# Kernel optimization log

Measured on AMD Instinct MI355X. Metric: run time of the kernel, lower is better.

Reference implementation:

```python
import jax, jax.numpy as jnp
import numpy as np

N, E, G = 50000, 800000, 64
DIN, HID, HEADS, L = 128, 128, 4, 3
CH = HID // HEADS  # 32
EPS = 1e-5


def seg_sum(d, ids, n):
    return jax.ops.segment_sum(d, ids, num_segments=n)


def seg_max(d, ids, n):
    return jax.ops.segment_max(d, ids, num_segments=n)


def seg_mean(d, ids, n):
    s = seg_sum(d, ids, n)
    c = seg_sum(jnp.ones((d.shape[0], 1), d.dtype), ids, n)
    return s / jnp.maximum(c, 1.0)


def setup_inputs() -> dict:
    key = jax.random.key(0)
    ks = jax.random.split(key, 24)
    p = lambda k, sh: jax.random.normal(k, sh, jnp.float32) * 0.05
    z = lambda *sh: jnp.zeros(sh, jnp.float32)
    return {
        'x': jax.random.normal(ks[0], (N, DIN), jnp.float32),
        'edge_index': jax.random.randint(ks[1], (2, E), 0, N),
        'batch': jnp.sort(jax.random.randint(ks[2], (N,), 0, G)),
        'proj_W': p(ks[3], (DIN, HID)), 'proj_b': z(HID),
        'gcn_W': p(ks[4], (L, HID, HID)), 'gcn_b': z(L, HID),
        'gat_W': p(ks[5], (L, HID, HID)),
        'gat_asrc': p(ks[6], (L, HEADS, CH)), 'gat_adst': p(ks[7], (L, HEADS, CH)),
        'gat_b': z(L, HID),
        'norm_w': jnp.ones((L, HID), jnp.float32), 'norm_b': z(L, HID),
        'norm_ms': jnp.ones((L, HID), jnp.float32),
        'hub_W1': p(ks[8], (HID, HID // 2)), 'hub_b1': z(HID // 2),
        'hub_W2': p(ks[9], (HID // 2, 4)), 'hub_b2': z(4),
        'att_W1': p(ks[10], (HID, HID // 2)), 'att_b1': z(HID // 2),
        'att_W2': p(ks[11], (HID // 2, 1)), 'att_b2': z(1),
        'pat_W1': p(ks[12], (HID * 2, HID)), 'pat_b1': z(HID),
        'pat_W2': p(ks[13], (HID, HID // 2)), 'pat_b2': z(HID // 2),
        'pat_W3': p(ks[14], (HID // 2, 8)), 'pat_b3': z(8),
        'cls_W1': p(ks[15], (HID + 12, HID)), 'cls_b1': z(HID),
        'cls_W2': p(ks[16], (HID, HID // 2)), 'cls_b2': z(HID // 2),
        'cls_W3': p(ks[17], (HID // 2, 2)), 'cls_b3': z(2),
    }


def _forward(fl, edge_index, batch):
    src, dst = edge_index[0], edge_index[1]
    loops = jnp.arange(N)
    s = jnp.concatenate([src, loops])  # with self-loops (GCN/GAT default)
    d = jnp.concatenate([dst, loops])

    x = fl['x'] @ fl['proj_W'] + fl['proj_b']  # [N, HID]

    # symmetric GCN normalization (shared across layers)
    deg = seg_sum(jnp.ones(s.shape[0], jnp.float32), d, N)
    dis = jnp.where(deg > 0, 1.0 / jnp.sqrt(deg), 0.0)
    coef = (dis[s] * dis[d])[:, None]  # [E+N, 1]

    for i in range(L):
        # GCNConv: out[dst] += norm * (x @ W)[src]
        h_gcn = seg_sum((x @ fl['gcn_W'][i])[s] * coef, d, N) + fl['gcn_b'][i]
        # GATConv (heads=4, concat), eval mode (no dropout)
        hh = (x @ fl['gat_W'][i]).reshape(N, HEADS, CH)
        a_s = (hh * fl['gat_asrc'][i]).sum(-1)  # [N, HEADS]
        a_d = (hh * fl['gat_adst'][i]).sum(-1)
        e = jax.nn.leaky_relu(a_s[s] + a_d[d], negative_slope=0.2)  # [E+N, HEADS]
        e = jnp.exp(e - seg_max(e, d, N)[d])
        alpha = e / seg_sum(e, d, N)[d]
        h_gat = seg_sum(hh[s] * alpha[:, :, None], d, N).reshape(N, HID) + fl['gat_b'][i]
        h = h_gcn + h_gat
        # GraphNorm: per-graph, per-feature
        mean = seg_mean(h, batch, G)
        out = h - fl['norm_ms'][i] * mean[batch]
        var = seg_mean(out * out, batch, G)
        out = out / jnp.sqrt(var[batch] + EPS)
        h = jax.nn.relu(fl['norm_w'][i] * out + fl['norm_b'][i])
        x = h if i == 0 else x + h

    # hub importance: normalized max degree per graph == 1.0 iff any degree > 0
    ones_e = jnp.ones(E, jnp.float32)
    node_deg = seg_sum(ones_e, src, N) + seg_sum(ones_e, dst, N)
    max_deg = seg_max(node_deg, batch, G)
    hub_importance = (max_deg > 0).astype(jnp.float32)

    hub_feat = jax.nn.relu(x @ fl['hub_W1'] + fl['hub_b1']) @ fl['hub_W2'] + fl['hub_b2']
    hub_pooled = seg_mean(hub_feat, batch, G)  # [G, 4]

    # attention pooling: softmax over ALL nodes (dim=0), then per-graph weighted sum
    w = jax.nn.relu(x @ fl['att_W1'] + fl['att_b1']) @ fl['att_W2'] + fl['att_b2']  # [N,1]
    w = jax.nn.softmax(w, axis=0)
    graph_emb = seg_sum(x * w, batch, G)  # [G, HID]

    pattern_emb = jnp.concatenate([seg_mean(x, batch, G), seg_max(x, batch, G)], axis=1)
    pf = jax.nn.relu(pattern_emb @ fl['pat_W1'] + fl['pat_b1'])
    pf = jax.nn.relu(pf @ fl['pat_W2'] + fl['pat_b2'])
    pattern_features = pf @ fl['pat_W3'] + fl['pat_b3']  # [G, 8]

    comb = jnp.concatenate([graph_emb, hub_pooled, pattern_features], axis=1)
    c = jax.nn.relu(comb @ fl['cls_W1'] + fl['cls_b1'])
    c = jax.nn.relu(c @ fl['cls_W2'] + fl['cls_b2'])
    logits = c @ fl['cls_W3'] + fl['cls_b3']  # [G, 2]
    return logits, hub_importance, graph_emb, hub_pooled, pattern_features


def reference(x, edge_index, batch, proj_W, proj_b, gcn_W, gcn_b, gat_W, gat_asrc,
              gat_adst, gat_b, norm_w, norm_b, norm_ms, hub_W1, hub_b1, hub_W2,
              hub_b2, att_W1, att_b1, att_W2, att_b2, pat_W1, pat_b1, pat_W2,
              pat_b2, pat_W3, pat_b3, cls_W1, cls_b1, cls_W2, cls_b2, cls_W3, cls_b3):
    fl = dict(x=x, proj_W=proj_W, proj_b=proj_b, gcn_W=gcn_W, gcn_b=gcn_b,
              gat_W=gat_W, gat_asrc=gat_asrc, gat_adst=gat_adst, gat_b=gat_b,
              norm_w=norm_w, norm_b=norm_b, norm_ms=norm_ms,
              hub_W1=hub_W1, hub_b1=hub_b1, hub_W2=hub_W2, hub_b2=hub_b2,
              att_W1=att_W1, att_b1=att_b1, att_W2=att_W2, att_b2=att_b2,
              pat_W1=pat_W1, pat_b1=pat_b1, pat_W2=pat_W2, pat_b2=pat_b2,
              pat_W3=pat_W3, pat_b3=pat_b3, cls_W1=cls_W1, cls_b1=cls_b1,
              cls_W2=cls_W2, cls_b2=cls_b2, cls_W3=cls_W3, cls_b3=cls_b3)
    return _forward(fl, edge_index, batch)
```

## Files before the change

### kernel.cpp

```cpp
#include <hip/hip_runtime.h>

#define NN 50000
#define NE 800000
#define NG 64
#define HID 128

typedef __attribute__((ext_vector_type(8))) short bf16x8;
typedef __attribute__((ext_vector_type(4))) float f32x4;

__device__ __forceinline__ unsigned short f2b(float f) {
  unsigned u = __float_as_uint(f);
  u += 0x7fffu + ((u >> 16) & 1u);
  return (unsigned short)(u >> 16);
}
__device__ __forceinline__ float b2f(unsigned short b) {
  return __uint_as_float(((unsigned)b) << 16);
}

__global__ void count_edges(const int* __restrict__ ei, int* __restrict__ cnt_dst,
                            int* __restrict__ cnt_src) {
  int e = blockIdx.x * 256 + threadIdx.x;
  if (e >= NE) return;
  atomicAdd(&cnt_src[ei[e]], 1);
  atomicAdd(&cnt_dst[ei[NE + e]], 1);
}

__global__ void compute_dis(const int* __restrict__ cnt_dst, float* __restrict__ dis) {
  int n = blockIdx.x * 256 + threadIdx.x;
  if (n >= NN) return;
  dis[n] = rsqrtf((float)(cnt_dst[n] + 1));
}

__global__ void scanA(const int* __restrict__ cnt, int* __restrict__ partial) {
  __shared__ int s[256];
  int t = threadIdx.x;
  int i = blockIdx.x * 256 + t;
  s[t] = (i < NN) ? cnt[i] : 0;
  __syncthreads();
  for (int off = 128; off; off >>= 1) {
    if (t < off) s[t] += s[t + off];
    __syncthreads();
  }
  if (!t) partial[blockIdx.x] = s[0];
}

__global__ void scanB(int* __restrict__ partial, int nb) {
  if (threadIdx.x == 0 && blockIdx.x == 0) {
    int acc = 0;
    for (int i = 0; i < nb; ++i) { int v = partial[i]; partial[i] = acc; acc += v; }
  }
}

__global__ void scanC(const int* __restrict__ cnt, const int* __restrict__ partial,
                      int* __restrict__ rowptr) {
  __shared__ int bufA[256], bufB[256];
  int t = threadIdx.x;
  int i = blockIdx.x * 256 + t;
  int v = (i < NN) ? cnt[i] : 0;
  bufA[t] = v;
  __syncthreads();
  int* src = bufA; int* dst = bufB;
  for (int off = 1; off < 256; off <<= 1) {
    int x = src[t];
    if (t >= off) x += src[t - off];
    dst[t] = x;
    __syncthreads();
    int* tmp = src; src = dst; dst = tmp;
  }
  int incl = src[t];
  if (i < NN) rowptr[i] = partial[blockIdx.x] + incl - v;
  if (i == NN - 1) rowptr[NN] = partial[blockIdx.x] + incl;
}

__global__ void fill_edges(const int* __restrict__ ei, const int* __restrict__ rowptr,
                           int* __restrict__ fillpos, int* __restrict__ col) {
  int e = blockIdx.x * 256 + threadIdx.x;
  if (e >= NE) return;
  int s = ei[e], d = ei[NE + e];
  int p = atomicAdd(&fillpos[d], 1);
  col[rowptr[d] + p] = s;
}

__global__ void graph_bounds(const int* __restrict__ batch, int* __restrict__ gstart) {
  int g = threadIdx.x;
  if (g > NG) return;
  int lo = 0, hi = NN;
  while (lo < hi) { int mid = (lo + hi) >> 1; if (batch[mid] < g) lo = mid + 1; else hi = mid; }
  gstart[g] = lo;
}

__global__ void prep_wfrag(const float* __restrict__ gcn_W, const float* __restrict__ gat_W,
                           unsigned short* __restrict__ F) {
  int l = blockIdx.y;
  int idx = blockIdx.x * 256 + threadIdx.x;
  int j = idx & 7, lane = (idx >> 3) & 63, t = idx >> 9;
  int ct = t >> 2, ks = t & 3;
  int k = ks * 32 + ((lane >> 4) << 3) + j;
  int c = (ct << 4) + (lane & 15);
  const float* W1 = gcn_W + (size_t)l * 16384;
  const float* W2 = gat_W + (size_t)l * 16384;
  F[(size_t)l * 32768 + idx] = f2b(W1[k * 128 + c]);
  F[(size_t)l * 32768 + 16384 + idx] = f2b(W2[k * 128 + c]);
}

__global__ void prep_frag1(const float* __restrict__ W, unsigned short* __restrict__ F) {
  int idx = blockIdx.x * 256 + threadIdx.x;
  int j = idx & 7, lane = (idx >> 3) & 63, t = idx >> 9;
  int ct = t >> 2, ks = t & 3;
  int k = ks * 32 + ((lane >> 4) << 3) + j;
  int c = (ct << 4) + (lane & 15);
  F[idx] = f2b(W[k * 128 + c]);
}

__global__ void prep_nodefrag(const float* __restrict__ hW1, const float* __restrict__ aW1,
                              unsigned short* __restrict__ F) {
  int idx = blockIdx.x * 256 + threadIdx.x;
  int j = idx & 7, lane = (idx >> 3) & 63, t = idx >> 9;
  int ct = t >> 2, ks = t & 3;
  int k = ks * 32 + ((lane >> 4) << 3) + j;
  int c = (ct << 4) + (lane & 15);
  float v = (c < 64) ? hW1[k * 64 + c] : aW1[k * 64 + (c - 64)];
  F[idx] = f2b(v);
}

__device__ __forceinline__ void load_a_frags(const float* __restrict__ xp, int lane,
                                             bf16x8 a[4]) {
#pragma unroll
  for (int ks = 0; ks < 4; ++ks) {
    int k0 = ks * 32 + ((lane >> 4) << 3);
    float4 u = *(const float4*)&xp[k0];
    float4 v = *(const float4*)&xp[k0 + 4];
    bf16x8 t;
    t[0] = (short)f2b(u.x); t[1] = (short)f2b(u.y); t[2] = (short)f2b(u.z); t[3] = (short)f2b(u.w);
    t[4] = (short)f2b(v.x); t[5] = (short)f2b(v.y); t[6] = (short)f2b(v.z); t[7] = (short)f2b(v.w);
    a[ks] = t;
  }
}

__global__ __launch_bounds__(256) void gemm_proj_mfma(
    const float* __restrict__ X, const unsigned short* __restrict__ F,
    const float* __restrict__ bias, float* __restrict__ Y, int nrows) {
  __shared__ float Ys[64 * 128];
  int tid = threadIdx.x;
  int w = tid >> 6, lane = tid & 63;
  int row0 = blockIdx.x * 64;
  int row = row0 + w * 16 + (lane & 15);
  const float* xp = (row < nrows) ? &X[(size_t)row * 128] : &X[0];
  bf16x8 a[4];
  load_a_frags(xp, lane, a);
  f32x4 acc[8];
#pragma unroll
  for (int ct = 0; ct < 8; ++ct) acc[ct] = (f32x4){0.f, 0.f, 0.f, 0.f};
#pragma unroll
  for (int ct = 0; ct < 8; ++ct) {
#pragma unroll
    for (int ks = 0; ks < 4; ++ks) {
      bf16x8 b = *(const bf16x8*)&F[((ct * 4 + ks) * 64 + lane) * 8];
      acc[ct] = __builtin_amdgcn_mfma_f32_16x16x32_bf16(a[ks], b, acc[ct], 0, 0, 0);
    }
  }
#pragma unroll
  for (int ct = 0; ct < 8; ++ct) {
    int c = (ct << 4) + (lane & 15);
    float bv = bias[c];
#pragma unroll
    for (int j = 0; j < 4; ++j) {
      int r = w * 16 + ((lane >> 4) << 2) + j;
      Ys[r * 128 + c] = acc[ct][j] + bv;
    }
  }
  __syncthreads();
  int nr = min(nrows - row0, 64);
  const float4* ys4 = (const float4*)Ys;
  float4* y4 = (float4*)(Y + (size_t)row0 * 128);
  for (int e = tid; e < nr * 32; e += 256) y4[e] = ys4[e];
}

__global__ __launch_bounds__(256) void gemm_dual_mfma(
    const float* __restrict__ X, const unsigned short* __restrict__ F1,
    const unsigned short* __restrict__ F2, const float* __restrict__ asrc,
    const float* __restrict__ adst, unsigned short* __restrict__ G,
    float* __restrict__ a_s, float* __restrict__ a_d, int nrows) {
  __shared__ unsigned short Gs[64 * 256];
  int tid = threadIdx.x;
  int w = tid >> 6, lane = tid & 63;
  int row0 = blockIdx.x * 64;
  int row = row0 + w * 16 + (lane & 15);
  const float* xp = (row < nrows) ? &X[(size_t)row * 128] : &X[0];
  bf16x8 a[4];
  load_a_frags(xp, lane, a);
  f32x4 acc1[8], acc2[8];
#pragma unroll
  for (int ct = 0; ct < 8; ++ct) {
    acc1[ct] = (f32x4){0.f, 0.f, 0.f, 0.f};
    acc2[ct] = (f32x4){0.f, 0.f, 0.f, 0.f};
  }
#pragma unroll
  for (int ct = 0; ct < 8; ++ct) {
#pragma unroll
    for (int ks = 0; ks < 4; ++ks) {
      int off = ((ct * 4 + ks) * 64 + lane) * 8;
      bf16x8 b1 = *(const bf16x8*)&F1[off];
      bf16x8 b2 = *(const bf16x8*)&F2[off];
      acc1[ct] = __builtin_amdgcn_mfma_f32_16x16x32_bf16(a[ks], b1, acc1[ct], 0, 0, 0);
      acc2[ct] = __builtin_amdgcn_mfma_f32_16x16x32_bf16(a[ks], b2, acc2[ct], 0, 0, 0);
    }
  }
#pragma unroll
  for (int ct = 0; ct < 8; ++ct) {
#pragma unroll
    for (int j = 0; j < 4; ++j) {
      int r = w * 16 + ((lane >> 4) << 2) + j;
      int c = (ct << 4) + (lane & 15);
      Gs[r * 256 + c] = f2b(acc1[ct][j]);
      Gs[r * 256 + 128 + c] = f2b(acc2[ct][j]);
    }
  }
  __syncthreads();
  int nr = min(nrows - row0, 64);
  const uint4* gs4 = (const uint4*)Gs;
  uint4* g4 = (uint4*)(G + (size_t)row0 * 256);
  for (int e = tid; e < nr * 32; e += 256) g4[e] = gs4[e];
  int f = 2 * lane;
  float as0 = asrc[f], as1 = asrc[f + 1];
  float ad0 = adst[f], ad1 = adst[f + 1];
  for (int i = 0; i < 16; ++i) {
    int r = w * 16 + i;
    int n = row0 + r;
    if (n >= nrows) break;
    ushort2 v = *(const ushort2*)&Gs[r * 256 + 128 + f];
    float x0 = b2f(v.x), x1 = b2f(v.y);
    float ps = x0 * as0 + x1 * as1;
    float pd = x0 * ad0 + x1 * ad1;
    ps += __shfl_xor(ps, 1); pd += __shfl_xor(pd, 1);
    ps += __shfl_xor(ps, 2); pd += __shfl_xor(pd, 2);
    ps += __shfl_xor(ps, 4); pd += __shfl_xor(pd, 4);
    ps += __shfl_xor(ps, 8); pd += __shfl_xor(pd, 8);
    if ((lane & 15) == 0) {
      int h = lane >> 4;
      a_s[n * 4 + h] = ps;
      a_d[n * 4 + h] = pd;
    }
  }
}

__global__ __launch_bounds__(256) void node_mlps_mfma(
    const float* __restrict__ x, const unsigned short* __restrict__ Fn,
    const float* __restrict__ hb1, const float* __restrict__ ab1,
    const float* __restrict__ hW2, const float* __restrict__ hb2,
    const float* __restrict__ aW2, const float* __restrict__ ab2,
    float* __restrict__ hub_feat, float* __restrict__ w_att) {
  __shared__ float Hs[64 * 133];
  int tid = threadIdx.x;
  int w = tid >> 6, lane = tid & 63;
  int row0 = blockIdx.x * 64;
  int row = row0 + w * 16 + (lane & 15);
  const float* xp = (row < NN) ? &x[(size_t)row * 128] : &x[0];
  bf16x8 a[4];
  load_a_frags(xp, lane, a);
  f32x4 acc[8];
#pragma unroll
  for (int ct = 0; ct < 8; ++ct) acc[ct] = (f32x4){0.f, 0.f, 0.f, 0.f};
#pragma unroll
  for (int ct = 0; ct < 8; ++ct) {
#pragma unroll
    for (int ks = 0; ks < 4; ++ks) {
      bf16x8 b = *(const bf16x8*)&Fn[((ct * 4 + ks) * 64 + lane) * 8];
      acc[ct] = __builtin_amdgcn_mfma_f32_16x16x32_bf16(a[ks], b, acc[ct], 0, 0, 0);
    }
  }
#pragma unroll
  for (int ct = 0; ct < 8; ++ct) {
    int c = (ct << 4) + (lane & 15);
    float bias = (c < 64) ? hb1[c] : ab1[c - 64];
#pragma unroll
    for (int j = 0; j < 4; ++j) {
      int r = w * 16 + ((lane >> 4) << 2) + j;
      float v = acc[ct][j] + bias;
      Hs[r * 133 + c] = v > 0.f ? v : 0.f;
    }
  }
  __syncthreads();
  int r = tid & 63, o = tid >> 6;
  int n = row0 + r;
  if (n < NN) {
    float d = hb2[o];
#pragma unroll 8
    for (int k = 0; k < 64; ++k) d += Hs[r * 133 + k] * hW2[k * 4 + o];
    hub_feat[n * 4 + o] = d;
    if (tid < 64) {
      float d2 = ab2[0];
#pragma unroll 8
      for (int k = 0; k < 64; ++k) d2 += Hs[r * 133 + 64 + k] * aW2[k];
      w_att[n] = d2;
    }
  }
}

__device__ __forceinline__ float lrelu(float v) { return v > 0.f ? v : 0.2f * v; }

__global__ __launch_bounds__(256) void edge_aggregate_p(
    const unsigned short* __restrict__ G, const float* __restrict__ a_s,
    const float* __restrict__ a_d, const float* __restrict__ dis,
    const int* __restrict__ rowptr, const int* __restrict__ col,
    const float* __restrict__ gcn_b, const float* __restrict__ gat_b,
    float* __restrict__ hout) {
  int n = blockIdx.x * 4 + (threadIdx.x >> 6);
  int lane = threadIdx.x & 63;
  int es = lane >> 4, fl = lane & 15;
  int h = fl >> 2;
  int f8 = fl << 3;
  int p0 = rowptr[n], p1 = rowptr[n + 1];
  int cnt = p1 - p0 + 1;
  float adh = a_d[n * 4 + h];
  float dn = dis[n];
  float ag[8] = {0.f, 0.f, 0.f, 0.f, 0.f, 0.f, 0.f, 0.f};
  float aa[8] = {0.f, 0.f, 0.f, 0.f, 0.f, 0.f, 0.f, 0.f};
  float ssum = 0.f;
#define EDGE_ACC(coef, eu, xv, hv)                          \
  do {                                                      \
    ag[0] += (coef)*__uint_as_float((xv).x << 16);          \
    ag[1] += (coef)*__uint_as_float((xv).x & 0xffff0000u);  \
    ag[2] += (coef)*__uint_as_float((xv).y << 16);          \
    ag[3] += (coef)*__uint_as_float((xv).y & 0xffff0000u);  \
    ag[4] += (coef)*__uint_as_float((xv).z << 16);          \
    ag[5] += (coef)*__uint_as_float((xv).z & 0xffff0000u);  \
    ag[6] += (coef)*__uint_as_float((xv).w << 16);          \
    ag[7] += (coef)*__uint_as_float((xv).w & 0xffff0000u);  \
    aa[0] += (eu)*__uint_as_float((hv).x << 16);            \
    aa[1] += (eu)*__uint_as_float((hv).x & 0xffff0000u);    \
    aa[2] += (eu)*__uint_as_float((hv).y << 16);            \
    aa[3] += (eu)*__uint_as_float((hv).y & 0xffff0000u);    \
    aa[4] += (eu)*__uint_as_float((hv).z << 16);            \
    aa[5] += (eu)*__uint_as_float((hv).z & 0xffff0000u);    \
    aa[6] += (eu)*__uint_as_float((hv).w << 16);            \
    aa[7] += (eu)*__uint_as_float((hv).w & 0xffff0000u);    \
  } while (0)
  int e = es;
  for (; e + 4 < cnt; e += 8) {
    int eB = e + 4;
    int srcA = (e < cnt - 1) ? col[p0 + e] : n;
    int srcB = (eB < cnt - 1) ? col[p0 + eB] : n;
    float coefA = dis[srcA] * dn, coefB = dis[srcB] * dn;
    float euA = __expf(lrelu(a_s[srcA * 4 + h] + adh));
    float euB = __expf(lrelu(a_s[srcB * 4 + h] + adh));
    uint4 xvA = *(const uint4*)&G[(size_t)srcA * 256 + f8];
    uint4 hvA = *(const uint4*)&G[(size_t)srcA * 256 + 128 + f8];
    uint4 xvB = *(const uint4*)&G[(size_t)srcB * 256 + f8];
    uint4 hvB = *(const uint4*)&G[(size_t)srcB * 256 + 128 + f8];
    ssum += euA + euB;
    EDGE_ACC(coefA, euA, xvA, hvA);
    EDGE_ACC(coefB, euB, xvB, hvB);
  }
  for (; e < cnt; e += 4) {
    int src = (e < cnt - 1) ? col[p0 + e] : n;
    float coef = dis[src] * dn;
    float eu = __expf(lrelu(a_s[src * 4 + h] + adh));
    uint4 xv = *(const uint4*)&G[(size_t)src * 256 + f8];
    uint4 hv = *(const uint4*)&G[(size_t)src * 256 + 128 + f8];
    ssum += eu;
    EDGE_ACC(coef, eu, xv, hv);
  }
#undef EDGE_ACC
#pragma unroll
  for (int j = 0; j < 8; ++j) {
    ag[j] += __shfl_xor(ag[j], 16); ag[j] += __shfl_xor(ag[j], 32);
    aa[j] += __shfl_xor(aa[j], 16); aa[j] += __shfl_xor(aa[j], 32);
  }
  ssum += __shfl_xor(ssum, 16); ssum += __shfl_xor(ssum, 32);
  if (es == 0) {
    float rs = 1.f / ssum;
    float4 gb0 = *(const float4*)&gcn_b[f8];
    float4 gb1 = *(const float4*)&gcn_b[f8 + 4];
    float4 tb0 = *(const float4*)&gat_b[f8];
    float4 tb1 = *(const float4*)&gat_b[f8 + 4];
    float4 o0, o1;
    o0.x = ag[0] + aa[0] * rs + gb0.x + tb0.x;
    o0.y = ag[1] + aa[1] * rs + gb0.y + tb0.y;
    o0.z = ag[2] + aa[2] * rs + gb0.z + tb0.z;
    o0.w = ag[3] + aa[3] * rs + gb0.w + tb0.w;
    o1.x = ag[4] + aa[4] * rs + gb1.x + tb1.x;
    o1.y = ag[5] + aa[5] * rs + gb1.y + tb1.y;
    o1.z = ag[6] + aa[6] * rs + gb1.z + tb1.z;
    o1.w = ag[7] + aa[7] * rs + gb1.w + tb1.w;
    *(float4*)&hout[n * 128 + f8] = o0;
    *(float4*)&hout[n * 128 + f8 + 4] = o1;
  }
}

__global__ __launch_bounds__(128) void graph_stats_par(
    const float* __restrict__ h, const int* __restrict__ batch,
    float* __restrict__ S1, float* __restrict__ S2) {
  int f = threadIdx.x;
  int n0 = blockIdx.x * 64;
  int n1 = min(n0 + 64, NN);
  int g = batch[n0];
  float s1 = 0.f, s2 = 0.f;
  for (int n = n0; n < n1; ++n) {
    int gn = batch[n];
    if (gn != g) {
      atomicAdd(&S1[g * 128 + f], s1);
      atomicAdd(&S2[g * 128 + f], s2);
      s1 = 0.f; s2 = 0.f; g = gn;
    }
    float v = h[n * 128 + f];
    s1 += v; s2 += v * v;
  }
  atomicAdd(&S1[g * 128 + f], s1);
  atomicAdd(&S2[g * 128 + f], s2);
}

__global__ __launch_bounds__(256) void graph_norm(
    const float* __restrict__ h, const int* __restrict__ batch,
    const int* __restrict__ gstart, const float* __restrict__ S1,
    const float* __restrict__ S2, const float* __restrict__ nw,
    const float* __restrict__ nb, const float* __restrict__ nms,
    float* __restrict__ x, int layer) {
  int idx = blockIdx.x * 256 + threadIdx.x;
  if (idx >= NN * 32) return;
  int n = idx >> 5, fq = (idx & 31) << 2;
  int g = batch[n];
  float c = fmaxf((float)(gstart[g + 1] - gstart[g]), 1.f);
  float rc = 1.f / c;
  float4 s1 = *(const float4*)&S1[g * 128 + fq];
  float4 s2 = *(const float4*)&S2[g * 128 + fq];
  float4 ms = *(const float4*)&nms[fq];
  float4 w = *(const float4*)&nw[fq];
  float4 b = *(const float4*)&nb[fq];
  float4 hv = *(const float4*)&h[(size_t)n * 128 + fq];
  float4 o;
#define GN1(X)                                                           \
  {                                                                      \
    float mean = s1.X * rc;                                              \
    float var = s2.X * rc - mean * mean * ms.X * (2.f - ms.X);           \
    var = fmaxf(var, 0.f);                                               \
    float ot = (hv.X - ms.X * mean) * rsqrtf(var + 1e-5f);               \
    float t = w.X * ot + b.X;                                            \
    o.X = t > 0.f ? t : 0.f;                                             \
  }
  GN1(x) GN1(y) GN1(z) GN1(w)
#undef GN1
  float4* xp = (float4*)&x[(size_t)n * 128 + fq];
  if (layer == 0) {
    *xp = o;
  } else {
    float4 xo = *xp;
    xo.x += o.x; xo.y += o.y; xo.z += o.z; xo.w += o.w;
    *xp = xo;
  }
}

__global__ void reduce_max1(const float* __restrict__ w, float* __restrict__ tmpM) {
  __shared__ float s[256];
  int t = threadIdx.x;
  float m = -1e30f;
  for (int i = blockIdx.x * 256 + t; i < NN; i += gridDim.x * 256) m = fmaxf(m, w[i]);
  s[t] = m;
  __syncthreads();
  for (int off = 128; off; off >>= 1) {
    if (t < off) s[t] = fmaxf(s[t], s[t + off]);
    __syncthreads();
  }
  if (!t) tmpM[blockIdx.x] = s[0];
}

__global__ void reduce_max2(const float* __restrict__ tmpM, float* __restrict__ scal) {
  __shared__ float s[256];
  int t = threadIdx.x;
  s[t] = tmpM[t];
  __syncthreads();
  for (int off = 128; off; off >>= 1) {
    if (t < off) s[t] = fmaxf(s[t], s[t + off]);
    __syncthreads();
  }
  if (!t) scal[0] = s[0];
}

__global__ void reduce_sum1(const float* __restrict__ w, const float* __restrict__ scal,
                            float* __restrict__ tmpS) {
  __shared__ float s[256];
  int t = threadIdx.x;
  float gmax = scal[0];
  float acc = 0.f;
  for (int i = blockIdx.x * 256 + t; i < NN; i += gridDim.x * 256) acc += __expf(w[i] - gmax);
  s[t] = acc;
  __syncthreads();
  for (int off = 128; off; off >>= 1) {
    if (t < off) s[t] += s[t + off];
    __syncthreads();
  }
  if (!t) tmpS[blockIdx.x] = s[0];
}

__global__ void reduce_sum2(const float* __restrict__ tmpS, float* __restrict__ scal) {
  __shared__ float s[256];
  int t = threadIdx.x;
  s[t] = tmpS[t];
  __syncthreads();
  for (int off = 128; off; off >>= 1) {
    if (t < off) s[t] += s[t + off];
    __syncthreads();
  }
  if (!t) scal[1] = s[0];
}

__global__ __launch_bounds__(128) void graph_pool_par(
    const float* __restrict__ x, const float* __restrict__ hub_feat,
    const float* __restrict__ w_att, const int* __restrict__ batch,
    const float* __restrict__ scal, float* __restrict__ Sx,
    unsigned* __restrict__ Mx, float* __restrict__ WSx, float* __restrict__ Shub) {
  int f = threadIdx.x;
  int n0 = blockIdx.x * 64;
  int n1 = min(n0 + 64, NN);
  float gmax = scal[0];
  int g = batch[n0];
  float sx = 0.f, wx = 0.f, mx = 0.f, sh = 0.f;
  for (int n = n0; n < n1; ++n) {
    int gn = batch[n];
    if (gn != g) {
      atomicAdd(&Sx[g * 128 + f], sx);
      atomicAdd(&WSx[g * 128 + f], wx);
      atomicMax(&Mx[g * 128 + f], __float_as_uint(mx));
      if (f < 4) atomicAdd(&Shub[g * 4 + f], sh);
      sx = 0.f; wx = 0.f; mx = 0.f; sh = 0.f; g = gn;
    }
    float xv = x[n * 128 + f];
    float ew = __expf(w_att[n] - gmax);
    sx += xv;
    wx += ew * xv;
    mx = fmaxf(mx, xv);
    if (f < 4) sh += hub_feat[n * 4 + f];
  }
  atomicAdd(&Sx[g * 128 + f], sx);
  atomicAdd(&WSx[g * 128 + f], wx);
  atomicMax(&Mx[g * 128 + f], __float_as_uint(mx));
  if (f < 4) atomicAdd(&Shub[g * 4 + f], sh);
}

__global__ __launch_bounds__(128) void finalize(
    const float* __restrict__ Sx, const float* __restrict__ Mx,
    const float* __restrict__ WSx, const float* __restrict__ Shub,
    const float* __restrict__ scal, const int* __restrict__ gstart,
    const int* __restrict__ cnt_src, const int* __restrict__ cnt_dst,
    const float* __restrict__ pW1, const float* __restrict__ pb1,
    const float* __restrict__ pW2, const float* __restrict__ pb2,
    const float* __restrict__ pW3, const float* __restrict__ pb3,
    const float* __restrict__ cW1, const float* __restrict__ cb1,
    const float* __restrict__ cW2, const float* __restrict__ cb2,
    const float* __restrict__ cW3, const float* __restrict__ cb3,
    float* __restrict__ out) {
  int g = blockIdx.x, t = threadIdx.x;
  __shared__ float pe[256], comb[140], buf1[128], buf2[64];
  __shared__ int snd[128];
  int s = gstart[g], e = gstart[g + 1];
  float c = fmaxf((float)(e - s), 1.f);
  int mdeg = 0;
  for (int n = s + t; n < e; n += 128) mdeg = max(mdeg, cnt_src[n] + cnt_dst[n]);
  snd[t] = mdeg;
  float* out_logits = out;
  float* out_hub = out + 128;
  float* out_ge = out + 192;
  float* out_hp = out + 192 + 8192;
  float* out_pf = out + 192 + 8192 + 256;
  float ge = WSx[g * 128 + t] / scal[1];
  out_ge[g * 128 + t] = ge;
  comb[t] = ge;
  pe[t] = Sx[g * 128 + t] / c;
  pe[128 + t] = Mx[g * 128 + t];
  if (t < 4) {
    float hp = Shub[g * 4 + t] / c;
    out_hp[g * 4 + t] = hp;
    comb[128 + t] = hp;
  }
  __syncthreads();
  for (int off = 64; off; off >>= 1) {
    if (t < off) snd[t] = max(snd[t], snd[t + off]);
    __syncthreads();
  }
  if (t == 0) out_hub[g] = (snd[0] > 0) ? 1.f : 0.f;
  float v = pb1[t];
  for (int k = 0; k < 256; ++k) v += pe[k] * pW1[k * 128 + t];
  buf1[t] = v > 0.f ? v : 0.f;
  __syncthreads();
  if (t < 64) {
    float v2 = pb2[t];
    for (int k = 0; k < 128; ++k) v2 += buf1[k] * pW2[k * 64 + t];
    buf2[t] = v2 > 0.f ? v2 : 0.f;
  }
  __syncthreads();
  if (t < 8) {
    float v3 = pb3[t];
    for (int k = 0; k < 64; ++k) v3 += buf2[k] * pW3[k * 8 + t];
    out_pf[g * 8 + t] = v3;
    comb[132 + t] = v3;
  }
  __syncthreads();
  float u = cb1[t];
  for (int k = 0; k < 140; ++k) u += comb[k] * cW1[k * 128 + t];
  buf1[t] = u > 0.f ? u : 0.f;
  __syncthreads();
  if (t < 64) {
    float u2 = cb2[t];
    for (int k = 0; k < 128; ++k) u2 += buf1[k] * cW2[k * 64 + t];
    buf2[t] = u2 > 0.f ? u2 : 0.f;
  }
  __syncthreads();
  if (t < 2) {
    float u3 = cb3[t];
    for (int k = 0; k < 64; ++k) u3 += buf2[k] * cW3[k * 2 + t];
    out_logits[g * 2 + t] = u3;
  }
}

extern "C" void kernel_launch(void* const* d_in, const int* in_sizes, int n_in,
                              void* d_out, int out_size, void* d_ws, size_t ws_size,
                              hipStream_t stream) {
  const float* x_in = (const float*)d_in[0];
  const int* ei = (const int*)d_in[1];
  const int* batch = (const int*)d_in[2];
  const float* proj_W = (const float*)d_in[3];
  const float* proj_b = (const float*)d_in[4];
  const float* gcn_W = (const float*)d_in[5];
  const float* gcn_b = (const float*)d_in[6];
  const float* gat_W = (const float*)d_in[7];
  const float* gat_as = (const float*)d_in[8];
  const float* gat_ad = (const float*)d_in[9];
  const float* gat_b = (const float*)d_in[10];
  const float* norm_w = (const float*)d_in[11];
  const float* norm_b = (const float*)d_in[12];
  const float* norm_ms = (const float*)d_in[13];
  const float* hub_W1 = (const float*)d_in[14];
  const float* hub_b1 = (const float*)d_in[15];
  const float* hub_W2 = (const float*)d_in[16];
  const float* hub_b2 = (const float*)d_in[17];
  const float* att_W1 = (const float*)d_in[18];
  const float* att_b1 = (const float*)d_in[19];
  const float* att_W2 = (const float*)d_in[20];
  const float* att_b2 = (const float*)d_in[21];
  const float* pat_W1 = (const float*)d_in[22];
  const float* pat_b1 = (const float*)d_in[23];
  const float* pat_W2 = (const float*)d_in[24];
  const float* pat_b2 = (const float*)d_in[25];
  const float* pat_W3 = (const float*)d_in[26];
  const float* pat_b3 = (const float*)d_in[27];
  const float* cls_W1 = (const float*)d_in[28];
  const float* cls_b1 = (const float*)d_in[29];
  const float* cls_W2 = (const float*)d_in[30];
  const float* cls_b2 = (const float*)d_in[31];
  const float* cls_W3 = (const float*)d_in[32];
  const float* cls_b3 = (const float*)d_in[33];
  float* out = (float*)d_out;

  char* ws = (char*)d_ws;
  auto fbuf = [&](size_t n) { float* p = (float*)ws; ws += ((n * 4 + 255) / 256) * 256; return p; };
  auto ibuf = [&](size_t n) { int* p = (int*)ws; ws += ((n * 4 + 255) / 256) * 256; return p; };

  float* x = fbuf((size_t)NN * 128);
  unsigned short* gath = (unsigned short*)fbuf((size_t)NN * 128);
  float* h = fbuf((size_t)NN * 128);
  unsigned short* wfrag = (unsigned short*)fbuf(3 * 32768 / 2);
  unsigned short* nfrag = (unsigned short*)fbuf(16384 / 2);
  unsigned short* pfrag = (unsigned short*)fbuf(16384 / 2);
  float* a_s = fbuf((size_t)NN * 4);
  float* a_d = fbuf((size_t)NN * 4);
  float* dis = fbuf(NN);
  float* w_att = fbuf(NN);
  float* hub_feat = fbuf((size_t)NN * 4);
  float* S1 = fbuf(NG * 128);
  float* S2 = fbuf(NG * 128);
  float* Sx = fbuf(NG * 128);
  float* Mx = fbuf(NG * 128);
  float* WSx = fbuf(NG * 128);
  float* Shub = fbuf(NG * 4);
  float* tmpM = fbuf(256);
  float* tmpS = fbuf(256);
  float* scal = fbuf(4);
  int* zero0 = ibuf(3 * NN);
  int* cnt_dst = zero0;
  int* cnt_src = zero0 + NN;
  int* fillpos = zero0 + 2 * NN;
  int* rowptr = ibuf(NN + 1);
  int* col = ibuf(NE);
  int* partial = ibuf(256);
  int* gstart = ibuf(NG + 1);

  const int NB = (NN + 255) / 256;
  const int NC = (NN + 63) / 64;
  const int GM = (NN + 63) / 64;

  hipMemsetAsync(zero0, 0, (size_t)3 * NN * 4, stream);
  count_edges<<<NE / 256, 256, 0, stream>>>(ei, cnt_dst, cnt_src);
  compute_dis<<<NB, 256, 0, stream>>>(cnt_dst, dis);
  scanA<<<NB, 256, 0, stream>>>(cnt_dst, partial);
  scanB<<<1, 64, 0, stream>>>(partial, NB);
  scanC<<<NB, 256, 0, stream>>>(cnt_dst, partial, rowptr);
  fill_edges<<<NE / 256, 256, 0, stream>>>(ei, rowptr, fillpos, col);
  graph_bounds<<<1, 128, 0, stream>>>(batch, gstart);
  prep_wfrag<<<dim3(64, 3), 256, 0, stream>>>(gcn_W, gat_W, wfrag);
  prep_nodefrag<<<64, 256, 0, stream>>>(hub_W1, att_W1, nfrag);
  prep_frag1<<<64, 256, 0, stream>>>(proj_W, pfrag);

  gemm_proj_mfma<<<GM, 256, 0, stream>>>(x_in, pfrag, proj_b, x, NN);

  for (int l = 0; l < 3; ++l) {
    gemm_dual_mfma<<<GM, 256, 0, stream>>>(x, wfrag + (size_t)l * 32768,
                                           wfrag + (size_t)l * 32768 + 16384,
                                           gat_as + l * 128, gat_ad + l * 128,
                                           gath, a_s, a_d, NN);
    edge_aggregate_p<<<NN / 4, 256, 0, stream>>>(gath, a_s, a_d, dis, rowptr, col,
                                                 gcn_b + l * 128, gat_b + l * 128, h);
    hipMemsetAsync(S1, 0, (size_t)2 * NG * 128 * 4, stream);
    graph_stats_par<<<NC, 128, 0, stream>>>(h, batch, S1, S2);
    graph_norm<<<(NN * 32 + 255) / 256, 256, 0, stream>>>(h, batch, gstart, S1, S2,
                                                          norm_w + l * 128, norm_b + l * 128,
                                                          norm_ms + l * 128, x, l);
  }

  node_mlps_mfma<<<GM, 256, 0, stream>>>(x, nfrag, hub_b1, att_b1, hub_W2, hub_b2,
                                         att_W2, att_b2, hub_feat, w_att);

  reduce_max1<<<256, 256, 0, stream>>>(w_att, tmpM);
  reduce_max2<<<1, 256, 0, stream>>>(tmpM, scal);
  reduce_sum1<<<256, 256, 0, stream>>>(w_att, scal, tmpS);
  reduce_sum2<<<1, 256, 0, stream>>>(tmpS, scal);

  hipMemsetAsync(Sx, 0, (size_t)(3 * NG * 128 + NG * 4) * 4, stream);
  graph_pool_par<<<NC, 128, 0, stream>>>(x, hub_feat, w_att, batch, scal,
                                         Sx, (unsigned*)Mx, WSx, Shub);

  finalize<<<NG, 128, 0, stream>>>(Sx, Mx, WSx, Shub, scal, gstart, cnt_src, cnt_dst,
                                   pat_W1, pat_b1, pat_W2, pat_b2, pat_W3, pat_b3,
                                   cls_W1, cls_b1, cls_W2, cls_b2, cls_W3, cls_b3, out);
}
```

Before: 602.7 us.

## Fuse setup kernels, keep bf16 activations, prescale GCN by dis, drop softmax max

Merges the dis computation into the scan, graph bounds into the scan-B kernel, and the three weight-fragment prep kernels into one launch. Graph norm and projection also write a bf16 copy of x, which the MFMA GEMMs read directly instead of converting fp32. The source-side GCN normalization is applied in the GEMM epilogue, removing a per-edge dis gather. Memsets move into kernels, and the attention softmax max-reduction is removed, which risks overflow if attention logits grow large.

```diff
diff --git a/kernel.cpp b/kernel.cpp
--- a/kernel.cpp
+++ b/kernel.cpp
@@ -25,17 +25,14 @@
   atomicAdd(&cnt_dst[ei[NE + e]], 1);
 }
 
-__global__ void compute_dis(const int* __restrict__ cnt_dst, float* __restrict__ dis) {
-  int n = blockIdx.x * 256 + threadIdx.x;
-  if (n >= NN) return;
-  dis[n] = rsqrtf((float)(cnt_dst[n] + 1));
-}
-
-__global__ void scanA(const int* __restrict__ cnt, int* __restrict__ partial) {
+__global__ void scanA_dis(const int* __restrict__ cnt, int* __restrict__ partial,
+                          float* __restrict__ dis) {
   __shared__ int s[256];
   int t = threadIdx.x;
   int i = blockIdx.x * 256 + t;
-  s[t] = (i < NN) ? cnt[i] : 0;
+  int v = (i < NN) ? cnt[i] : 0;
+  if (i < NN) dis[i] = rsqrtf((float)(v + 1));
+  s[t] = v;
   __syncthreads();
   for (int off = 128; off; off >>= 1) {
     if (t < off) s[t] += s[t + off];
@@ -44,10 +41,18 @@
   if (!t) partial[blockIdx.x] = s[0];
 }
 
-__global__ void scanB(int* __restrict__ partial, int nb) {
-  if (threadIdx.x == 0 && blockIdx.x == 0) {
+__global__ void scanB_bounds(int* __restrict__ partial, int nb,
+                             const int* __restrict__ batch, int* __restrict__ gstart) {
+  int t = threadIdx.x;
+  if (t == 0) {
     int acc = 0;
     for (int i = 0; i < nb; ++i) { int v = partial[i]; partial[i] = acc; acc += v; }
+  }
+  if (t >= 1 && t <= NG + 1) {
+    int g = t - 1;
+    int lo = 0, hi = NN;
+    while (lo < hi) { int mid = (lo + hi) >> 1; if (batch[mid] < g) lo = mid + 1; else hi = mid; }
+    gstart[g] = lo;
   }
 }
 
@@ -81,50 +86,29 @@
   col[rowptr[d] + p] = s;
 }
 
-__global__ void graph_bounds(const int* __restrict__ batch, int* __restrict__ gstart) {
-  int g = threadIdx.x;
-  if (g > NG) return;
-  int lo = 0, hi = NN;
-  while (lo < hi) { int mid = (lo + hi) >> 1; if (batch[mid] < g) lo = mid + 1; else hi = mid; }
-  gstart[g] = lo;
-}
-
-__global__ void prep_wfrag(const float* __restrict__ gcn_W, const float* __restrict__ gat_W,
-                           unsigned short* __restrict__ F) {
-  int l = blockIdx.y;
+__global__ void prep_all(const float* __restrict__ gcn_W, const float* __restrict__ gat_W,
+                         const float* __restrict__ hW1, const float* __restrict__ aW1,
+                         const float* __restrict__ projW, unsigned short* __restrict__ wfrag,
+                         unsigned short* __restrict__ nfrag, unsigned short* __restrict__ pfrag) {
+  int m = blockIdx.y;
   int idx = blockIdx.x * 256 + threadIdx.x;
   int j = idx & 7, lane = (idx >> 3) & 63, t = idx >> 9;
   int ct = t >> 2, ks = t & 3;
   int k = ks * 32 + ((lane >> 4) << 3) + j;
   int c = (ct << 4) + (lane & 15);
-  const float* W1 = gcn_W + (size_t)l * 16384;
-  const float* W2 = gat_W + (size_t)l * 16384;
-  F[(size_t)l * 32768 + idx] = f2b(W1[k * 128 + c]);
-  F[(size_t)l * 32768 + 16384 + idx] = f2b(W2[k * 128 + c]);
-}
-
-__global__ void prep_frag1(const float* __restrict__ W, unsigned short* __restrict__ F) {
-  int idx = blockIdx.x * 256 + threadIdx.x;
-  int j = idx & 7, lane = (idx >> 3) & 63, t = idx >> 9;
-  int ct = t >> 2, ks = t & 3;
-  int k = ks * 32 + ((lane >> 4) << 3) + j;
-  int c = (ct << 4) + (lane & 15);
-  F[idx] = f2b(W[k * 128 + c]);
-}
-
-__global__ void prep_nodefrag(const float* __restrict__ hW1, const float* __restrict__ aW1,
-                              unsigned short* __restrict__ F) {
-  int idx = blockIdx.x * 256 + threadIdx.x;
-  int j = idx & 7, lane = (idx >> 3) & 63, t = idx >> 9;
-  int ct = t >> 2, ks = t & 3;
-  int k = ks * 32 + ((lane >> 4) << 3) + j;
-  int c = (ct << 4) + (lane & 15);
-  float v = (c < 64) ? hW1[k * 64 + c] : aW1[k * 64 + (c - 64)];
-  F[idx] = f2b(v);
-}
-
-__device__ __forceinline__ void load_a_frags(const float* __restrict__ xp, int lane,
-                                             bf16x8 a[4]) {
+  if (m < 3) {
+    wfrag[(size_t)m * 32768 + idx] = f2b(gcn_W[(size_t)m * 16384 + k * 128 + c]);
+    wfrag[(size_t)m * 32768 + 16384 + idx] = f2b(gat_W[(size_t)m * 16384 + k * 128 + c]);
+  } else if (m == 3) {
+    float v = (c < 64) ? hW1[k * 64 + c] : aW1[k * 64 + (c - 64)];
+    nfrag[idx] = f2b(v);
+  } else {
+    pfrag[idx] = f2b(projW[k * 128 + c]);
+  }
+}
+
+__device__ __forceinline__ void load_a_frags_f32(const float* __restrict__ xp, int lane,
+                                                 bf16x8 a[4]) {
 #pragma unroll
   for (int ks = 0; ks < 4; ++ks) {
     int k0 = ks * 32 + ((lane >> 4) << 3);
@@ -137,9 +121,19 @@
   }
 }
 
+__device__ __forceinline__ void load_a_frags_b16(const unsigned short* __restrict__ xp,
+                                                 int lane, bf16x8 a[4]) {
+#pragma unroll
+  for (int ks = 0; ks < 4; ++ks) {
+    int k0 = ks * 32 + ((lane >> 4) << 3);
+    a[ks] = *(const bf16x8*)&xp[k0];
+  }
+}
+
 __global__ __launch_bounds__(256) void gemm_proj_mfma(
     const float* __restrict__ X, const unsigned short* __restrict__ F,
-    const float* __restrict__ bias, float* __restrict__ Y, int nrows) {
+    const float* __restrict__ bias, float* __restrict__ Y,
+    unsigned short* __restrict__ YB, int nrows) {
   __shared__ float Ys[64 * 128];
   int tid = threadIdx.x;
   int w = tid >> 6, lane = tid & 63;
@@ -147,7 +141,7 @@
   int row = row0 + w * 16 + (lane & 15);
   const float* xp = (row < nrows) ? &X[(size_t)row * 128] : &X[0];
   bf16x8 a[4];
-  load_a_frags(xp, lane, a);
+  load_a_frags_f32(xp, lane, a);
   f32x4 acc[8];
 #pragma unroll
   for (int ct = 0; ct < 8; ++ct) acc[ct] = (f32x4){0.f, 0.f, 0.f, 0.f};
@@ -173,22 +167,30 @@
   int nr = min(nrows - row0, 64);
   const float4* ys4 = (const float4*)Ys;
   float4* y4 = (float4*)(Y + (size_t)row0 * 128);
-  for (int e = tid; e < nr * 32; e += 256) y4[e] = ys4[e];
+  ushort4* yb4 = (ushort4*)(YB + (size_t)row0 * 128);
+  for (int e = tid; e < nr * 32; e += 256) {
+    float4 v = ys4[e];
+    y4[e] = v;
+    ushort4 b;
+    b.x = f2b(v.x); b.y = f2b(v.y); b.z = f2b(v.z); b.w = f2b(v.w);
+    yb4[e] = b;
+  }
 }
 
 __global__ __launch_bounds__(256) void gemm_dual_mfma(
-    const float* __restrict__ X, const unsigned short* __restrict__ F1,
+    const unsigned short* __restrict__ XB, const unsigned short* __restrict__ F1,
     const unsigned short* __restrict__ F2, const float* __restrict__ asrc,
-    const float* __restrict__ adst, unsigned short* __restrict__ G,
-    float* __restrict__ a_s, float* __restrict__ a_d, int nrows) {
+    const float* __restrict__ adst, const float* __restrict__ dis,
+    unsigned short* __restrict__ G, float* __restrict__ a_s, float* __restrict__ a_d,
+    int nrows) {
   __shared__ unsigned short Gs[64 * 256];
   int tid = threadIdx.x;
   int w = tid >> 6, lane = tid & 63;
   int row0 = blockIdx.x * 64;
   int row = row0 + w * 16 + (lane & 15);
-  const float* xp = (row < nrows) ? &X[(size_t)row * 128] : &X[0];
+  const unsigned short* xp = (row < nrows) ? &XB[(size_t)row * 128] : &XB[0];
   bf16x8 a[4];
-  load_a_frags(xp, lane, a);
+  load_a_frags_b16(xp, lane, a);
   f32x4 acc1[8], acc2[8];
 #pragma unroll
   for (int ct = 0; ct < 8; ++ct) {
@@ -206,13 +208,19 @@
       acc2[ct] = __builtin_amdgcn_mfma_f32_16x16x32_bf16(a[ks], b2, acc2[ct], 0, 0, 0);
     }
   }
+  float dv[4];
+#pragma unroll
+  for (int j = 0; j < 4; ++j) {
+    int gr = row0 + w * 16 + ((lane >> 4) << 2) + j;
+    dv[j] = dis[gr < nrows ? gr : 0];
+  }
 #pragma unroll
   for (int ct = 0; ct < 8; ++ct) {
 #pragma unroll
     for (int j = 0; j < 4; ++j) {
       int r = w * 16 + ((lane >> 4) << 2) + j;
       int c = (ct << 4) + (lane & 15);
-      Gs[r * 256 + c] = f2b(acc1[ct][j]);
+      Gs[r * 256 + c] = f2b(acc1[ct][j] * dv[j]);
       Gs[r * 256 + 128 + c] = f2b(acc2[ct][j]);
     }
   }
@@ -245,7 +253,7 @@
 }
 
 __global__ __launch_bounds__(256) void node_mlps_mfma(
-    const float* __restrict__ x, const unsigned short* __restrict__ Fn,
+    const unsigned short* __restrict__ XB, const unsigned short* __restrict__ Fn,
     const float* __restrict__ hb1, const float* __restrict__ ab1,
     const float* __restrict__ hW2, const float* __restrict__ hb2,
     const float* __restrict__ aW2, const float* __restrict__ ab2,
@@ -255,9 +263,9 @@
   int w = tid >> 6, lane = tid & 63;
   int row0 = blockIdx.x * 64;
   int row = row0 + w * 16 + (lane & 15);
-  const float* xp = (row < NN) ? &x[(size_t)row * 128] : &x[0];
+  const unsigned short* xp = (row < NN) ? &XB[(size_t)row * 128] : &XB[0];
   bf16x8 a[4];
-  load_a_frags(xp, lane, a);
+  load_a_frags_b16(xp, lane, a);
   f32x4 acc[8];
 #pragma unroll
   for (int ct = 0; ct < 8; ++ct) acc[ct] = (f32x4){0.f, 0.f, 0.f, 0.f};
@@ -304,7 +312,10 @@
     const float* __restrict__ a_d, const float* __restrict__ dis,
     const int* __restrict__ rowptr, const int* __restrict__ col,
     const float* __restrict__ gcn_b, const float* __restrict__ gat_b,
-    float* __restrict__ hout) {
+    float* __restrict__ hout, float* __restrict__ S1z) {
+  if (blockIdx.x == 0) {
+    for (int i = threadIdx.x; i < 2 * NG * 128; i += 256) S1z[i] = 0.f;
+  }
   int n = blockIdx.x * 4 + (threadIdx.x >> 6);
   int lane = threadIdx.x & 63;
   int es = lane >> 4, fl = lane & 15;
@@ -317,16 +328,16 @@
   float ag[8] = {0.f, 0.f, 0.f, 0.f, 0.f, 0.f, 0.f, 0.f};
   float aa[8] = {0.f, 0.f, 0.f, 0.f, 0.f, 0.f, 0.f, 0.f};
   float ssum = 0.f;
-#define EDGE_ACC(coef, eu, xv, hv)                          \
+#define EDGE_ACC(eu, xv, hv)                                \
   do {                                                      \
-    ag[0] += (coef)*__uint_as_float((xv).x << 16);          \
-    ag[1] += (coef)*__uint_as_float((xv).x & 0xffff0000u);  \
-    ag[2] += (coef)*__uint_as_float((xv).y << 16);          \
-    ag[3] += (coef)*__uint_as_float((xv).y & 0xffff0000u);  \
-    ag[4] += (coef)*__uint_as_float((xv).z << 16);          \
-    ag[5] += (coef)*__uint_as_float((xv).z & 0xffff0000u);  \
-    ag[6] += (coef)*__uint_as_float((xv).w << 16);          \
-    ag[7] += (coef)*__uint_as_float((xv).w & 0xffff0000u);  \
+    ag[0] += __uint_as_float((xv).x << 16);                 \
+    ag[1] += __uint_as_float((xv).x & 0xffff0000u);         \
+    ag[2] += __uint_as_float((xv).y << 16);                 \
+    ag[3] += __uint_as_float((xv).y & 0xffff0000u);         \
+    ag[4] += __uint_as_float((xv).z << 16);                 \
+    ag[5] += __uint_as_float((xv).z & 0xffff0000u);         \
+    ag[6] += __uint_as_float((xv).w << 16);                 \
+    ag[7] += __uint_as_float((xv).w & 0xffff0000u);         \
     aa[0] += (eu)*__uint_as_float((hv).x << 16);            \
     aa[1] += (eu)*__uint_as_float((hv).x & 0xffff0000u);    \
     aa[2] += (eu)*__uint_as_float((hv).y << 16);            \
@@ -341,7 +352,6 @@
     int eB = e + 4;
     int srcA = (e < cnt - 1) ? col[p0 + e] : n;
     int srcB = (eB < cnt - 1) ? col[p0 + eB] : n;
-    float coefA = dis[srcA] * dn, coefB = dis[srcB] * dn;
     float euA = __expf(lrelu(a_s[srcA * 4 + h] + adh));
     float euB = __expf(lrelu(a_s[srcB * 4 + h] + adh));
     uint4 xvA = *(const uint4*)&G[(size_t)srcA * 256 + f8];
@@ -349,17 +359,16 @@
     uint4 xvB = *(const uint4*)&G[(size_t)srcB * 256 + f8];
     uint4 hvB = *(const uint4*)&G[(size_t)srcB * 256 + 128 + f8];
     ssum += euA + euB;
-    EDGE_ACC(coefA, euA, xvA, hvA);
-    EDGE_ACC(coefB, euB, xvB, hvB);
+    EDGE_ACC(euA, xvA, hvA);
+    EDGE_ACC(euB, xvB, hvB);
   }
   for (; e < cnt; e += 4) {
     int src = (e < cnt - 1) ? col[p0 + e] : n;
-    float coef = dis[src] * dn;
     float eu = __expf(lrelu(a_s[src * 4 + h] + adh));
     uint4 xv = *(const uint4*)&G[(size_t)src * 256 + f8];
     uint4 hv = *(const uint4*)&G[(size_t)src * 256 + 128 + f8];
     ssum += eu;
-    EDGE_ACC(coef, eu, xv, hv);
+    EDGE_ACC(eu, xv, hv);
   }
 #undef EDGE_ACC
 #pragma unroll
@@ -375,14 +384,14 @@
     float4 tb0 = *(const float4*)&gat_b[f8];
     float4 tb1 = *(const float4*)&gat_b[f8 + 4];
     float4 o0, o1;
-    o0.x = ag[0] + aa[0] * rs + gb0.x + tb0.x;
-    o0.y = ag[1] + aa[1] * rs + gb0.y + tb0.y;
-    o0.z = ag[2] + aa[2] * rs + gb0.z + tb0.z;
-    o0.w = ag[3] + aa[3] * rs + gb0.w + tb0.w;
-    o1.x = ag[4] + aa[4] * rs + gb1.x + tb1.x;
-    o1.y = ag[5] + aa[5] * rs + gb1.y + tb1.y;
-    o1.z = ag[6] + aa[6] * rs + gb1.z + tb1.z;
-    o1.w = ag[7] + aa[7] * rs + gb1.w + tb1.w;
+    o0.x = ag[0] * dn + aa[0] * rs + gb0.x + tb0.x;
+    o0.y = ag[1] * dn + aa[1] * rs + gb0.y + tb0.y;
+    o0.z = ag[2] * dn + aa[2] * rs + gb0.z + tb0.z;
+    o0.w = ag[3] * dn + aa[3] * rs + gb0.w + tb0.w;
+    o1.x = ag[4] * dn + aa[4] * rs + gb1.x + tb1.x;
+    o1.y = ag[5] * dn + aa[5] * rs + gb1.y + tb1.y;
+    o1.z = ag[6] * dn + aa[6] * rs + gb1.z + tb1.z;
+    o1.w = ag[7] * dn + aa[7] * rs + gb1.w + tb1.w;
     *(float4*)&hout[n * 128 + f8] = o0;
     *(float4*)&hout[n * 128 + f8 + 4] = o1;
   }
@@ -415,7 +424,7 @@
     const int* __restrict__ gstart, const float* __restrict__ S1,
     const float* __restrict__ S2, const float* __restrict__ nw,
     const float* __restrict__ nb, const float* __restrict__ nms,
-    float* __restrict__ x, int layer) {
+    float* __restrict__ x, unsigned short* __restrict__ xb, int layer) {
   int idx = blockIdx.x * 256 + threadIdx.x;
   if (idx >= NN * 32) return;
   int n = idx >> 5, fq = (idx & 31) << 2;
@@ -441,48 +450,28 @@
   GN1(x) GN1(y) GN1(z) GN1(w)
 #undef GN1
   float4* xp = (float4*)&x[(size_t)n * 128 + fq];
+  float4 xo;
   if (layer == 0) {
-    *xp = o;
+    xo = o;
   } else {
-    float4 xo = *xp;
+    xo = *xp;
     xo.x += o.x; xo.y += o.y; xo.z += o.z; xo.w += o.w;
-    *xp = xo;
-  }
-}
-
-__global__ void reduce_max1(const float* __restrict__ w, float* __restrict__ tmpM) {
+  }
+  *xp = xo;
+  ushort4 bo;
+  bo.x = f2b(xo.x); bo.y = f2b(xo.y); bo.z = f2b(xo.z); bo.w = f2b(xo.w);
+  *(ushort4*)&xb[(size_t)n * 128 + fq] = bo;
+}
+
+__global__ void reduce_sum1(const float* __restrict__ w, float* __restrict__ tmpS,
+                            float* __restrict__ poolZ, int zcount) {
   __shared__ float s[256];
   int t = threadIdx.x;
-  float m = -1e30f;
-  for (int i = blockIdx.x * 256 + t; i < NN; i += gridDim.x * 256) m = fmaxf(m, w[i]);
-  s[t] = m;
-  __syncthreads();
-  for (int off = 128; off; off >>= 1) {
-    if (t < off) s[t] = fmaxf(s[t], s[t + off]);
-    __syncthreads();
-  }
-  if (!t) tmpM[blockIdx.x] = s[0];
-}
-
-__global__ void reduce_max2(const float* __restrict__ tmpM, float* __restrict__ scal) {
-  __shared__ float s[256];
-  int t = threadIdx.x;
-  s[t] = tmpM[t];
-  __syncthreads();
-  for (int off = 128; off; off >>= 1) {
-    if (t < off) s[t] = fmaxf(s[t], s[t + off]);
-    __syncthreads();
-  }
-  if (!t) scal[0] = s[0];
-}
-
-__global__ void reduce_sum1(const float* __restrict__ w, const float* __restrict__ scal,
-                            float* __restrict__ tmpS) {
-  __shared__ float s[256];
-  int t = threadIdx.x;
-  float gmax = scal[0];
+  if (blockIdx.x == 0) {
+    for (int i = t; i < zcount; i += 256) poolZ[i] = 0.f;
+  }
   float acc = 0.f;
-  for (int i = blockIdx.x * 256 + t; i < NN; i += gridDim.x * 256) acc += __expf(w[i] - gmax);
+  for (int i = blockIdx.x * 256 + t; i < NN; i += gridDim.x * 256) acc += __expf(w[i]);
   s[t] = acc;
   __syncthreads();
   for (int off = 128; off; off >>= 1) {
@@ -507,12 +496,11 @@
 __global__ __launch_bounds__(128) void graph_pool_par(
     const float* __restrict__ x, const float* __restrict__ hub_feat,
     const float* __restrict__ w_att, const int* __restrict__ batch,
-    const float* __restrict__ scal, float* __restrict__ Sx,
-    unsigned* __restrict__ Mx, float* __restrict__ WSx, float* __restrict__ Shub) {
+    float* __restrict__ Sx, unsigned* __restrict__ Mx, float* __restrict__ WSx,
+    float* __restrict__ Shub) {
   int f = threadIdx.x;
   int n0 = blockIdx.x * 64;
   int n1 = min(n0 + 64, NN);
-  float gmax = scal[0];
   int g = batch[n0];
   float sx = 0.f, wx = 0.f, mx = 0.f, sh = 0.f;
   for (int n = n0; n < n1; ++n) {
@@ -525,7 +513,7 @@
       sx = 0.f; wx = 0.f; mx = 0.f; sh = 0.f; g = gn;
     }
     float xv = x[n * 128 + f];
-    float ew = __expf(w_att[n] - gmax);
+    float ew = __expf(w_att[n]);
     sx += xv;
     wx += ew * xv;
     mx = fmaxf(mx, xv);
@@ -656,6 +644,7 @@
   auto ibuf = [&](size_t n) { int* p = (int*)ws; ws += ((n * 4 + 255) / 256) * 256; return p; };
 
   float* x = fbuf((size_t)NN * 128);
+  unsigned short* xb = (unsigned short*)fbuf((size_t)NN * 64);
   unsigned short* gath = (unsigned short*)fbuf((size_t)NN * 128);
   float* h = fbuf((size_t)NN * 128);
   unsigned short* wfrag = (unsigned short*)fbuf(3 * 32768 / 2);
@@ -672,7 +661,6 @@
   float* Mx = fbuf(NG * 128);
   float* WSx = fbuf(NG * 128);
   float* Shub = fbuf(NG * 4);
-  float* tmpM = fbuf(256);
   float* tmpS = fbuf(256);
   float* scal = fbuf(4);
   int* zero0 = ibuf(3 * NN);
@@ -690,42 +678,35 @@
 
   hipMemsetAsync(zero0, 0, (size_t)3 * NN * 4, stream);
   count_edges<<<NE / 256, 256, 0, stream>>>(ei, cnt_dst, cnt_src);
-  compute_dis<<<NB, 256, 0, stream>>>(cnt_dst, dis);
-  scanA<<<NB, 256, 0, stream>>>(cnt_dst, partial);
-  scanB<<<1, 64, 0, stream>>>(partial, NB);
+  scanA_dis<<<NB, 256, 0, stream>>>(cnt_dst, partial, dis);
+  scanB_bounds<<<1, 128, 0, stream>>>(partial, NB, batch, gstart);
   scanC<<<NB, 256, 0, stream>>>(cnt_dst, partial, rowptr);
   fill_edges<<<NE / 256, 256, 0, stream>>>(ei, rowptr, fillpos, col);
-  graph_bounds<<<1, 128, 0, stream>>>(batch, gstart);
-  prep_wfrag<<<dim3(64, 3), 256, 0, stream>>>(gcn_W, gat_W, wfrag);
-  prep_nodefrag<<<64, 256, 0, stream>>>(hub_W1, att_W1, nfrag);
-  prep_frag1<<<64, 256, 0, stream>>>(proj_W, pfrag);
-
-  gemm_proj_mfma<<<GM, 256, 0, stream>>>(x_in, pfrag, proj_b, x, NN);
+  prep_all<<<dim3(64, 5), 256, 0, stream>>>(gcn_W, gat_W, hub_W1, att_W1, proj_W,
+                                            wfrag, nfrag, pfrag);
+
+  gemm_proj_mfma<<<GM, 256, 0, stream>>>(x_in, pfrag, proj_b, x, xb, NN);
 
   for (int l = 0; l < 3; ++l) {
-    gemm_dual_mfma<<<GM, 256, 0, stream>>>(x, wfrag + (size_t)l * 32768,
+    gemm_dual_mfma<<<GM, 256, 0, stream>>>(xb, wfrag + (size_t)l * 32768,
                                            wfrag + (size_t)l * 32768 + 16384,
-                                           gat_as + l * 128, gat_ad + l * 128,
+                                           gat_as + l * 128, gat_ad + l * 128, dis,
                                            gath, a_s, a_d, NN);
     edge_aggregate_p<<<NN / 4, 256, 0, stream>>>(gath, a_s, a_d, dis, rowptr, col,
-                                                 gcn_b + l * 128, gat_b + l * 128, h);
-    hipMemsetAsync(S1, 0, (size_t)2 * NG * 128 * 4, stream);
+                                                 gcn_b + l * 128, gat_b + l * 128, h, S1);
     graph_stats_par<<<NC, 128, 0, stream>>>(h, batch, S1, S2);
     graph_norm<<<(NN * 32 + 255) / 256, 256, 0, stream>>>(h, batch, gstart, S1, S2,
                                                           norm_w + l * 128, norm_b + l * 128,
-                                                          norm_ms + l * 128, x, l);
-  }
-
-  node_mlps_mfma<<<GM, 256, 0, stream>>>(x, nfrag, hub_b1, att_b1, hub_W2, hub_b2,
+                                                          norm_ms + l * 128, x, xb, l);
+  }
+
+  node_mlps_mfma<<<GM, 256, 0, stream>>>(xb, nfrag, hub_b1, att_b1, hub_W2, hub_b2,
                                          att_W2, att_b2, hub_feat, w_att);
 
-  reduce_max1<<<256, 256, 0, stream>>>(w_att, tmpM);
-  reduce_max2<<<1, 256, 0, stream>>>(tmpM, scal);
-  reduce_sum1<<<256, 256, 0, stream>>>(w_att, scal, tmpS);
+  reduce_sum1<<<256, 256, 0, stream>>>(w_att, tmpS, Sx, 3 * NG * 128 + NG * 4);
   reduce_sum2<<<1, 256, 0, stream>>>(tmpS, scal);
 
-  hipMemsetAsync(Sx, 0, (size_t)(3 * NG * 128 + NG * 4) * 4, stream);
-  graph_pool_par<<<NC, 128, 0, stream>>>(x, hub_feat, w_att, batch, scal,
+  graph_pool_par<<<NC, 128, 0, stream>>>(x, hub_feat, w_att, batch,
                                          Sx, (unsigned*)Mx, WSx, Shub);
 
   finalize<<<NG, 128, 0, stream>>>(Sx, Mx, WSx, Shub, scal, gstart, cnt_src, cnt_dst,
```

Result: no change. 598.5 us (-0.7%).
